# Kernel tuning notes

Hardware: AMD Instinct MI355X
Metric: run time of the kernel (lower is better)

Reference implementation:

```python
import jax, jax.numpy as jnp
import numpy as np

WS = (6, 12, 12)
STRIDE = (2, 2, 2)
NHEAD = 8
NPF = 32


def _pos_embed(Dm, Hm, Wm, pw):
    # Sine 3D position embedding, normalized, then 1x1x1 conv proj (pw: (C, 6*NPF)).
    eps = 1e-6
    two_pi = np.float32(2.0 * np.pi)
    z = jnp.arange(Dm, dtype=jnp.float32) / (Dm - 1 + eps) * two_pi
    y = jnp.arange(Hm, dtype=jnp.float32) / (Hm - 1 + eps) * two_pi
    x = jnp.arange(Wm, dtype=jnp.float32) / (Wm - 1 + eps) * two_pi
    zz, yy, xx = jnp.meshgrid(z, y, x, indexing='ij')
    dim_t = jnp.float32(10000.0) ** (jnp.arange(NPF, dtype=jnp.float32) / NPF)
    def emb(p):
        p = p[..., None] / dim_t                       # (D,H,W,NPF)
        return jnp.stack([jnp.sin(p), jnp.cos(p)], axis=-1).reshape(p.shape[:-1] + (2 * NPF,))
    pos = jnp.concatenate([emb(zz), emb(yy), emb(xx)], axis=-1)  # (D,H,W,6*NPF)
    return jnp.einsum('dhwf,cf->cdhw', pos, pw)        # (C,D,H,W)


def _pad_to_multiple(x, ws):
    B, C, D, H, W = x.shape
    pd, ph, pw = (-D) % ws[0], (-H) % ws[1], (-W) % ws[2]
    if pd or ph or pw:
        x = jnp.pad(x, ((0, 0), (0, 0), (0, pd), (0, ph), (0, pw)))
    return x


def _match(x, tgt):
    x = x[:, :, :tgt[0], :tgt[1], :tgt[2]]
    pd, ph, pw = tgt[0] - x.shape[2], tgt[1] - x.shape[3], tgt[2] - x.shape[4]
    if pd or ph or pw:
        x = jnp.pad(x, ((0, 0), (0, 0), (0, pd), (0, ph), (0, pw)))
    return x


def _partition(x, ws):
    # (B,C,D,H,W) -> (B, Nw, L, C) window tokens
    B, C, D, H, W = x.shape
    wd, wh, ww = ws
    x = x.reshape(B, C, D // wd, wd, H // wh, wh, W // ww, ww)
    x = x.transpose(0, 2, 4, 6, 3, 5, 7, 1)  # B,Dg,Hg,Wg,wd,wh,ww,C
    return x.reshape(B, (D // wd) * (H // wh) * (W // ww), wd * wh * ww, C)


def _reverse(tok, grid, ws, B, C):
    Dg, Hg, Wg = grid
    wd, wh, ww = ws
    x = tok.reshape(B, Dg, Hg, Wg, wd, wh, ww, C)
    x = x.transpose(0, 7, 1, 4, 2, 5, 3, 6)
    return x.reshape(B, C, Dg * wd, Hg * wh, Wg * ww)


def _wavelet_low_high(x):
    # Depthwise Haar DWT, kernel 2, stride 2 (D,H,W even). Returns LLL and sum of 7 high bands.
    B, C, D, H, W = x.shape
    s = np.float32(1.0 / np.sqrt(2.0))
    t = x.reshape(B, C, D // 2, 2, H // 2, 2, W // 2, 2)
    zL = (t[:, :, :, 0] + t[:, :, :, 1]) * s
    zH = (t[:, :, :, 1] - t[:, :, :, 0]) * s
    def sy(u):
        return (u[:, :, :, :, 0] + u[:, :, :, :, 1]) * s, (u[:, :, :, :, 1] - u[:, :, :, :, 0]) * s
    def sw(u):
        return (u[..., 0] + u[..., 1]) * s, (u[..., 1] - u[..., 0]) * s
    LL_, LH_ = sy(zL)
    HL_, HH_ = sy(zH)
    LLL, LLH = sw(LL_)
    LHL, LHH = sw(LH_)
    HLL, HLH = sw(HL_)
    HHL, HHH = sw(HH_)
    return LLL, LLH + LHL + LHH + HLL + HLH + HHL + HHH


def _forward(query_map, memory_map, pos_w, l_w1, l_b1, l_w2, l_b2,
             g_w1, g_b1, g_w2, g_b2, in_w, in_b, out_w, out_b, ln_w, ln_b):
    B, C, D, H, W = query_map.shape
    wd, wh, ww = WS
    sd, sh, sw_ = STRIDE
    q_pad = _pad_to_multiple(query_map, WS)
    m_pad = _pad_to_multiple(memory_map, WS)
    Dp, Hp, Wp = q_pad.shape[2:]
    qpos = _pos_embed(Dp, Hp, Wp, pos_w)[None]          # (1,C,Dp,Hp,Wp)
    # frequency-only KV pre (wavelet + MSCM gating)
    low, high = _wavelet_low_high(m_pad)
    Dk, Hk, Wk = low.shape[2:]
    low_t = low.reshape(B, C, -1).transpose(0, 2, 1)    # (B,Nk,C)
    high_t = high.reshape(B, C, -1).transpose(0, 2, 1)
    xm = high_t + low_t
    g = xm.mean(axis=1, keepdims=True)
    loc = jnp.maximum(xm @ l_w1.T + l_b1, 0.0) @ l_w2.T + l_b2
    glo = jnp.maximum(g @ g_w1.T + g_b1, 0.0) @ g_w2.T + g_b2
    wgate = jax.nn.sigmoid(loc + glo)
    fre = wgate * high_t + low_t
    kv_map = fre.transpose(0, 2, 1).reshape(B, C, Dk, Hk, Wk)
    kpos = _pos_embed(Dk, Hk, Wk, pos_w)[None]
    k_ws = (wd // sd, wh // sh, ww // sw_)
    nD, nH, nW = Dp // wd, Hp // wh, Wp // ww
    tgt = (nD * k_ws[0], nH * k_ws[1], nW * k_ws[2])
    kv_map = _match(kv_map, tgt)
    kpos = _match(kpos, tgt)
    q_tok = _partition(q_pad, WS)        # (B,Nw,Lq,C)
    qp_tok = _partition(qpos, WS)        # (1,Nw,Lq,C) broadcast over batch
    k_tok = _partition(kv_map, k_ws)     # (B,Nw,Lk,C)
    kp_tok = _partition(kpos, k_ws)
    qin = q_tok + qp_tok
    kin = k_tok + kp_tok
    dh = C // NHEAD
    Wq, Wk_, Wv = in_w[:C], in_w[C:2 * C], in_w[2 * C:]
    bq, bk, bv = in_b[:C], in_b[C:2 * C], in_b[2 * C:]
    Nw, Lq, Lk = q_tok.shape[1], q_tok.shape[2], k_tok.shape[2]
    q = (qin @ Wq.T + bq).reshape(B, Nw, Lq, NHEAD, dh)
    k = (kin @ Wk_.T + bk).reshape(B, Nw, Lk, NHEAD, dh)
    v = (k_tok @ Wv.T + bv).reshape(B, Nw, Lk, NHEAD, dh)
    scale = np.float32(1.0 / np.sqrt(dh))
    att = jax.nn.softmax(jnp.einsum('bnqhd,bnkhd->bnhqk', q, k) * scale, axis=-1)
    o = jnp.einsum('bnhqk,bnkhd->bnqhd', att, v).reshape(B, Nw, Lq, C)
    o = o @ out_w.T + out_b
    res = q_tok + o
    mu = res.mean(-1, keepdims=True)
    var = res.var(-1, keepdims=True)
    res = (res - mu) * jax.lax.rsqrt(var + 1e-5) * ln_w + ln_b
    out = _reverse(res, (nD, nH, nW), WS, B, C)
    return out[:, :, :D, :H, :W]


def setup_inputs() -> dict:
    key = jax.random.key(0)
    ks = jax.random.split(key, 9)
    C = 96
    shp = (1, C, 24, 96, 96)
    def w(k, s, sc=0.05):
        return jax.random.normal(k, s, jnp.float32) * sc
    return {
        'query_map': jax.random.normal(ks[0], shp, jnp.float32),
        'memory_map': jax.random.normal(ks[1], shp, jnp.float32),
        'pos_w': w(ks[2], (C, 6 * NPF)),
        'l_w1': w(ks[3], (C, C)), 'l_b1': jnp.zeros((C,), jnp.float32),
        'l_w2': w(ks[4], (C, C)), 'l_b2': jnp.zeros((C,), jnp.float32),
        'g_w1': w(ks[5], (C, C)), 'g_b1': jnp.zeros((C,), jnp.float32),
        'g_w2': w(ks[6], (C, C)), 'g_b2': jnp.zeros((C,), jnp.float32),
        'in_w': w(ks[7], (3 * C, C)), 'in_b': jnp.zeros((3 * C,), jnp.float32),
        'out_w': w(ks[8], (C, C)), 'out_b': jnp.zeros((C,), jnp.float32),
        'ln_w': jnp.ones((C,), jnp.float32), 'ln_b': jnp.zeros((C,), jnp.float32),
    }


def reference(query_map, memory_map, pos_w, l_w1, l_b1, l_w2, l_b2,
              g_w1, g_b1, g_w2, g_b2, in_w, in_b, out_w, out_b, ln_w, ln_b):
    return _forward(query_map, memory_map, pos_w, l_w1, l_b1, l_w2, l_b2,
                    g_w1, g_b1, g_w2, g_b2, in_w, in_b, out_w, out_b, ln_w, ln_b)
```

## Files before the change

kernel.cpp:

```cpp
#include <hip/hip_runtime.h>
#include <math.h>


using short8 = __attribute__((ext_vector_type(8))) short;
using f32x4  = __attribute__((ext_vector_type(4))) float;

__device__ __forceinline__ unsigned short f2bf(float f) {
  unsigned u = __builtin_bit_cast(unsigned, f);
  unsigned r = u + 0x7fffu + ((u >> 16) & 1u);
  return (unsigned short)(r >> 16);
}
__device__ __forceinline__ unsigned cvtpk(float a, float b) {
  unsigned r;
  asm("v_cvt_pk_bf16_f32 %0, %1, %2" : "=v"(r) : "v"(a), "v"(b));
  return r;
}
__device__ __forceinline__ short8 mk8(unsigned a, unsigned b, unsigned c, unsigned d) {
  union { unsigned u[4]; short8 s; } x;
  x.u[0] = a; x.u[1] = b; x.u[2] = c; x.u[3] = d;
  return x.s;
}

#define OFFB_TAB   0u
#define OFFB_GSUM  124416u
#define OFFB_GLO   124800u
#define OFFB_XM    125184u
#define OFFB_LOW   10742016u
#define OFFB_WQ    21358848u
#define OFFB_WK    21377280u
#define OFFB_WV    21395712u
#define OFFB_KP    21414144u
#define OFFB_VT    28754176u
#define OFFB_WOP   37142784u
#define MEMSET_OFF 21414144u
#define MEMSET_LEN 15753216u

__global__ void k_pos(const float* __restrict__ pos_w, float* __restrict__ tab) {
  int idx = blockIdx.x * 256 + threadIdx.x;
  if (idx >= 324 * 96) return;
  int c = idx % 96, p = idx / 96;
  int Dm, fo, pl;
  if (p < 24)       { Dm = 24; fo = 0;   pl = p; }
  else if (p < 120) { Dm = 96; fo = 64;  pl = p - 24; }
  else if (p < 216) { Dm = 96; fo = 128; pl = p - 120; }
  else if (p < 228) { Dm = 12; fo = 0;   pl = p - 216; }
  else if (p < 276) { Dm = 48; fo = 64;  pl = p - 228; }
  else              { Dm = 48; fo = 128; pl = p - 276; }
  float pos = (float)pl / ((float)(Dm - 1) + 1e-6f) * 6.2831853071795864769f;
  float acc = 0.f;
  for (int i = 0; i < 32; ++i) {
    float inv = powf(10000.f, -(float)i / 32.f);
    float a = pos * inv;
    acc += sinf(a) * pos_w[c * 192 + fo + 2 * i] + cosf(a) * pos_w[c * 192 + fo + 2 * i + 1];
  }
  tab[p * 96 + c] = acc;
}

__global__ void k_wprep(const float* __restrict__ in_w, const float* __restrict__ out_w,
                        unsigned short* __restrict__ wq, unsigned short* __restrict__ wk,
                        unsigned short* __restrict__ wv, unsigned short* __restrict__ wop2) {
  int i = blockIdx.x * 256 + threadIdx.x;
  if (i < 9216) {
    wq[i] = f2bf(in_w[i]);
    wk[i] = f2bf(in_w[9216 + i]);
    wv[i] = f2bf(in_w[18432 + i]);
    int co = i / 96, ci = i % 96;
    int hh = ci / 12, dd = ci % 12;
    wop2[co * 128 + (hh >> 1) * 32 + (dd >> 2) * 8 + (hh & 1) * 4 + (dd & 3)] = f2bf(out_w[i]);
  }
}

__global__ void k_wav(const float* __restrict__ mem, float* __restrict__ xm_g,
                      float* __restrict__ low_g, float* __restrict__ gsum) {
  __shared__ float sxm[96][49];
  __shared__ float slow[96][49];
  int dk = blockIdx.x / 48, hk = blockIdx.x % 48;
  int tid = threadIdx.x;
  for (int idx = tid; idx < 96 * 48; idx += 256) {
    int wk = idx % 48, c = idx / 48;
    const float* p = mem + (((size_t)c * 24 + 2 * dk) * 96 + 2 * hk) * 96 + 2 * wk;
    float s = p[0] + p[1] + p[96] + p[97];
    const float* p2 = p + 96 * 96;
    float x111 = p2[97];
    s += p2[0] + p2[1] + p2[96] + x111;
    sxm[c][wk] = 2.8284271247461903f * x111;
    slow[c][wk] = 0.35355339059327373f * s;
  }
  __syncthreads();
  int n0 = (dk * 48 + hk) * 48;
  for (int idx = tid; idx < 96 * 48; idx += 256) {
    int c = idx % 96, t = idx / 96;
    xm_g[(size_t)(n0 + t) * 96 + c] = sxm[c][t];
    low_g[(size_t)(n0 + t) * 96 + c] = slow[c][t];
  }
  if (tid < 96) {
    float a = 0.f;
    for (int t = 0; t < 48; ++t) a += sxm[tid][t];
    atomicAdd(&gsum[tid], a);
  }
}

__global__ void k_glo(const float* __restrict__ gsum, const float* __restrict__ g_w1,
                      const float* __restrict__ g_b1, const float* __restrict__ g_w2,
                      const float* __restrict__ g_b2, float* __restrict__ glo) {
  __shared__ float sg[96], sh[96];
  int t = threadIdx.x;
  if (t < 96) sg[t] = gsum[t] * (1.f / 27648.f);
  __syncthreads();
  if (t < 96) {
    float a = g_b1[t];
    for (int i = 0; i < 96; ++i) a += sg[i] * g_w1[t * 96 + i];
    sh[t] = fmaxf(a, 0.f);
  }
  __syncthreads();
  if (t < 96) {
    float a = g_b2[t];
    for (int i = 0; i < 96; ++i) a += sh[i] * g_w2[t * 96 + i];
    glo[t] = a;
  }
}

__global__ __launch_bounds__(512) void k_gate(
    const float* xm_g, const float* __restrict__ low_g,
    const float* __restrict__ l_w1, const float* __restrict__ l_b1,
    const float* __restrict__ l_w2, const float* __restrict__ l_b2,
    const float* __restrict__ glo, float* fre) {
  __shared__ float sxm[64][97];
  __shared__ float sH[64][97];
  __shared__ float sW1[96][97];
  __shared__ float sW2[96][97];
  __shared__ float sb1[96], sb2[96], sglo[96];
  int tid = threadIdx.x;
  int n0 = blockIdx.x * 64;
  for (int idx = tid; idx < 64 * 96; idx += 512) {
    int c = idx % 96, t = idx / 96;
    sxm[t][c] = xm_g[(size_t)(n0 + t) * 96 + c];
  }
  for (int idx = tid; idx < 96 * 96; idx += 512) {
    int ci = idx % 96, co = idx / 96;
    sW1[co][ci] = l_w1[idx];
    sW2[co][ci] = l_w2[idx];
  }
  if (tid < 96) { sb1[tid] = l_b1[tid]; sb2[tid] = l_b2[tid]; sglo[tid] = glo[tid]; }
  __syncthreads();
  for (int idx = tid; idx < 64 * 96; idx += 512) {
    int co = idx % 96, t = idx / 96;
    float a = sb1[co];
    for (int ci = 0; ci < 96; ++ci) a += sxm[t][ci] * sW1[co][ci];
    sH[t][co] = fmaxf(a, 0.f);
  }
  __syncthreads();
  for (int idx = tid; idx < 64 * 96; idx += 512) {
    int co = idx % 96, t = idx / 96;
    float a = sb2[co];
    for (int ci = 0; ci < 96; ++ci) a += sH[t][ci] * sW2[co][ci];
    float wg = 1.f / (1.f + expf(-(a + sglo[co])));
    size_t off = (size_t)(n0 + t) * 96 + co;
    float lo = low_g[off];
    fre[off] = wg * (sxm[t][co] - lo) + lo;
  }
}

__global__ __launch_bounds__(256) void k_kv2(
    const float* __restrict__ fre, const float* __restrict__ tab,
    const unsigned short* __restrict__ wk, const unsigned short* __restrict__ wv,
    const float* __restrict__ in_b,
    unsigned short* __restrict__ kp2, unsigned short* __restrict__ vtp) {
  __shared__ unsigned short sKin[112 * 104];
  __shared__ unsigned short sVin[112 * 104];
  __shared__ unsigned short sVt[4 * 96 * 18];
  int tid = threadIdx.x, nw = blockIdx.x;
  int dg = nw >> 6, hg = (nw >> 3) & 7, wg = nw & 7;
  for (int idx = tid; idx < 108 * 48; idx += 256) {
    int row = idx % 108, cop = idx / 108;
    int ld = row / 36, lh = (row / 6) % 6, lw = row % 6;
    int dk = dg * 3 + ld, hk = hg * 6 + lh, wk_ = wg * 6 + lw;
    int n = (dk * 48 + hk) * 48 + wk_;
    int co = cop * 2;
    float f0 = fre[(size_t)n * 96 + co], f1 = fre[(size_t)n * 96 + co + 1];
    float p0 = tab[20736 + dk * 96 + co] + tab[21888 + hk * 96 + co] + tab[26496 + wk_ * 96 + co];
    float p1 = tab[20736 + dk * 96 + co + 1] + tab[21888 + hk * 96 + co + 1] + tab[26496 + wk_ * 96 + co + 1];
    *(unsigned*)(&sKin[row * 104 + co]) = (unsigned)f2bf(f0 + p0) | ((unsigned)f2bf(f1 + p1) << 16);
    *(unsigned*)(&sVin[row * 104 + co]) = (unsigned)f2bf(f0) | ((unsigned)f2bf(f1) << 16);
  }
  __syncthreads();
  int wave = tid >> 6, lane = tid & 63, l15 = lane & 15, g = lane >> 4;
  for (int mtk = wave; mtk < 7; mtk += 4) {
    f32x4 DK[6], DV[6];
    #pragma unroll
    for (int nt = 0; nt < 6; ++nt) { DK[nt] = f32x4{0.f,0.f,0.f,0.f}; DV[nt] = f32x4{0.f,0.f,0.f,0.f}; }
    #pragma unroll
    for (int ks = 0; ks < 3; ++ks) {
      short8 ak = *(const short8*)(&sKin[(mtk * 16 + l15) * 104 + ks * 32 + g * 8]);
      short8 av = *(const short8*)(&sVin[(mtk * 16 + l15) * 104 + ks * 32 + g * 8]);
      #pragma unroll
      for (int nt = 0; nt < 6; ++nt) {
        short8 bk = *(const short8*)(&wk[(nt * 16 + l15) * 96 + ks * 32 + g * 8]);
        short8 bv = *(const short8*)(&wv[(nt * 16 + l15) * 96 + ks * 32 + g * 8]);
        DK[nt] = __builtin_amdgcn_mfma_f32_16x16x32_bf16(ak, bk, DK[nt], 0, 0, 0);
        DV[nt] = __builtin_amdgcn_mfma_f32_16x16x32_bf16(av, bv, DV[nt], 0, 0, 0);
      }
    }
    #pragma unroll
    for (int nt = 0; nt < 6; ++nt) {
      int co = nt * 16 + l15;
      float bk_ = in_b[96 + co], bv_ = in_b[192 + co];
      #pragma unroll
      for (int r = 0; r < 4; ++r) {
        int row = g * 4 + r;
        int kk = mtk * 16 + row;
        float vk = DK[nt][r] + bk_;
        float vk2 = __shfl_xor(vk, 1);
        if (!(l15 & 1) && kk < 108) {
          unsigned pk = (unsigned)f2bf(vk) | ((unsigned)f2bf(vk2) << 16);
          *(unsigned*)(&kp2[((size_t)(nw * 8 + co / 12) * 112 + kk) * 16 + co % 12]) = pk;
        }
        float vv = DV[nt][r] + bv_;
        sVt[wave * 1728 + co * 18 + row] = f2bf(vv);
      }
    }
    asm volatile("s_waitcnt lgkmcnt(0)" ::: "memory");
    int cnt = (mtk == 6) ? 12 : 16;
    for (int co = lane; co < 96; co += 64) {
      int hh = co / 12, dd = co % 12;
      size_t vrowb = ((size_t)(nw * 8 + hh) * 16 + dd) * 128;
      for (int kk2 = 0; kk2 < cnt; kk2 += 2) {
        unsigned v = *(const unsigned*)(&sVt[wave * 1728 + co * 18 + kk2]);
        int p = (mtk >> 1) * 32 + (kk2 >> 2) * 8 + (mtk & 1) * 4 + (kk2 & 3);
        *(unsigned*)(&vtp[vrowb + p]) = v;
      }
    }
  }
}

__device__ __forceinline__ f32x4 proc_head(
    const unsigned short* qtile, const unsigned short* kb, const unsigned short* vb,
    int h, int lane, int l15, int g) {
  short8 bq = short8{0,0,0,0,0,0,0,0};
  if (lane < 32) bq = *(const short8*)(&qtile[l15 * 136 + h * 16 + g * 8]);
  short8 ak[7];
  #pragma unroll
  for (int nt = 0; nt < 7; ++nt) {
    ak[nt] = short8{0,0,0,0,0,0,0,0};
    if (lane < 32) ak[nt] = *(const short8*)(&kb[((size_t)h * 112 + nt * 16 + l15) * 16 + g * 8]);
  }
  f32x4 S[7];
  #pragma unroll
  for (int nt = 0; nt < 7; ++nt)
    S[nt] = __builtin_amdgcn_mfma_f32_16x16x32_bf16(ak[nt], bq, f32x4{0.f,0.f,0.f,0.f}, 0, 0, 0);
  float mx = -3e38f;
  #pragma unroll
  for (int nt = 0; nt < 6; ++nt) {
    #pragma unroll
    for (int r = 0; r < 4; ++r) mx = fmaxf(mx, S[nt][r]);
  }
  if (g < 3) {
    #pragma unroll
    for (int r = 0; r < 4; ++r) mx = fmaxf(mx, S[6][r]);
  }
  mx = fmaxf(mx, __shfl_xor(mx, 16));
  mx = fmaxf(mx, __shfl_xor(mx, 32));
  float sum = 0.f;
  #pragma unroll
  for (int nt = 0; nt < 7; ++nt) {
    #pragma unroll
    for (int r = 0; r < 4; ++r) {
      float e = __expf(S[nt][r] - mx);
      if (nt == 6 && g == 3) e = 0.f;
      S[nt][r] = e;
      sum += e;
    }
  }
  sum += __shfl_xor(sum, 16);
  sum += __shfl_xor(sum, 32);
  float inv = 1.f / sum;
  short8 av[4];
  #pragma unroll
  for (int ks = 0; ks < 4; ++ks)
    av[ks] = *(const short8*)(&vb[((size_t)h * 16 + l15) * 128 + ks * 32 + g * 8]);
  f32x4 o = f32x4{0.f, 0.f, 0.f, 0.f};
  #pragma unroll
  for (int ks = 0; ks < 4; ++ks) {
    unsigned w0 = cvtpk(S[2 * ks][0], S[2 * ks][1]);
    unsigned w1 = cvtpk(S[2 * ks][2], S[2 * ks][3]);
    unsigned w2 = 0, w3 = 0;
    if (ks < 3) {
      w2 = cvtpk(S[2 * ks + 1][0], S[2 * ks + 1][1]);
      w3 = cvtpk(S[2 * ks + 1][2], S[2 * ks + 1][3]);
    }
    short8 pa = mk8(w0, w1, w2, w3);
    o = __builtin_amdgcn_mfma_f32_16x16x32_bf16(av[ks], pa, o, 0, 0, 0);
  }
  o[0] *= inv; o[1] *= inv; o[2] *= inv; o[3] *= inv;
  return o;
}

__global__ __launch_bounds__(256, 2) void k_att4(
    const float* __restrict__ query, const float* __restrict__ tab,
    const unsigned short* __restrict__ kp2, const unsigned short* __restrict__ vtp,
    const unsigned short* __restrict__ wq, const unsigned short* __restrict__ wop2,
    const float* __restrict__ in_b, const float* __restrict__ out_b,
    const float* __restrict__ ln_w, const float* __restrict__ ln_b,
    float* __restrict__ out) {
  __shared__ __align__(16) unsigned char smem[34816];
  int tid = threadIdx.x;
  int nw = blockIdx.x, part = blockIdx.y;
  int dg = nw >> 6, hg = (nw >> 3) & 7, wg = nw & 7;
  int wave = tid >> 6, lane = tid & 63, l15 = lane & 15, g = lane >> 4;
  unsigned char* wbase = smem + wave * 8704;
  unsigned short* qtile = (unsigned short*)wbase;
  unsigned short* sPq   = qtile + 2176;
  int wid = part * 4 + wave;

  for (int c = lane; c < 544; c += 64)
    *(int4*)(wbase + c * 16) = int4{0, 0, 0, 0};
  asm volatile("s_waitcnt lgkmcnt(0)" ::: "memory");

  const float scale = 0.28867513459481287f;
  float biasq[6];
  #pragma unroll
  for (int nt = 0; nt < 6; ++nt) biasq[nt] = in_b[nt * 16 + l15];
  const unsigned short* kb = kp2 + (size_t)nw * 8 * 112 * 16;
  const unsigned short* vb = vtp + (size_t)nw * 8 * 16 * 128;

  for (int mt = wid; mt < 54; mt += 16) {
    for (int c = lane; c < 16 * 48; c += 64) {
      int row = c & 15, cop = c >> 4;
      int co = cop * 2;
      int l = mt * 16 + row;
      int ld = l / 144, lh = (l / 12) % 12, lw = l % 12;
      int d = dg * 6 + ld, h = hg * 12 + lh, w = wg * 12 + lw;
      size_t qoff = (((size_t)co * 24 + d) * 96 + h) * 96 + w;
      float v0 = query[qoff] + tab[d * 96 + co] + tab[2304 + h * 96 + co] + tab[11520 + w * 96 + co];
      float v1 = query[qoff + 221184] + tab[d * 96 + co + 1] + tab[2304 + h * 96 + co + 1] + tab[11520 + w * 96 + co + 1];
      *(unsigned*)(&sPq[row * 136 + co]) = (unsigned)f2bf(v0) | ((unsigned)f2bf(v1) << 16);
    }
    asm volatile("s_waitcnt lgkmcnt(0)" ::: "memory");
    {
      f32x4 QD[6];
      #pragma unroll
      for (int nt = 0; nt < 6; ++nt) QD[nt] = f32x4{0.f, 0.f, 0.f, 0.f};
      #pragma unroll
      for (int ks = 0; ks < 3; ++ks) {
        short8 a = *(const short8*)(&sPq[l15 * 136 + ks * 32 + g * 8]);
        #pragma unroll
        for (int nt = 0; nt < 6; ++nt) {
          short8 bw = *(const short8*)(&wq[(nt * 16 + l15) * 96 + ks * 32 + g * 8]);
          QD[nt] = __builtin_amdgcn_mfma_f32_16x16x32_bf16(a, bw, QD[nt], 0, 0, 0);
        }
      }
      #pragma unroll
      for (int nt = 0; nt < 6; ++nt) {
        int co = nt * 16 + l15;
        #pragma unroll
        for (int r = 0; r < 4; ++r) {
          float v = (QD[nt][r] + biasq[nt]) * scale;
          float v2 = __shfl_xor(v, 1);
          if (!(l15 & 1)) {
            int row = g * 4 + r;
            unsigned pk = (unsigned)f2bf(v) | ((unsigned)f2bf(v2) << 16);
            *(unsigned*)(&qtile[row * 136 + (co / 12) * 16 + co % 12]) = pk;
          }
        }
      }
    }
    asm volatile("s_waitcnt lgkmcnt(0)" ::: "memory");
    f32x4 R[6];
    #pragma unroll
    for (int nt = 0; nt < 6; ++nt) R[nt] = f32x4{0.f, 0.f, 0.f, 0.f};
    #pragma unroll
    for (int hp = 0; hp < 4; ++hp) {
      f32x4 oA = proc_head(qtile, kb, vb, 2 * hp, lane, l15, g);
      f32x4 oB = proc_head(qtile, kb, vb, 2 * hp + 1, lane, l15, g);
      short8 pb = mk8(cvtpk(oA[0], oA[1]), cvtpk(oA[2], oA[3]),
                      cvtpk(oB[0], oB[1]), cvtpk(oB[2], oB[3]));
      #pragma unroll
      for (int nt = 0; nt < 6; ++nt) {
        short8 aw = *(const short8*)(&wop2[(nt * 16 + l15) * 128 + hp * 32 + g * 8]);
        R[nt] = __builtin_amdgcn_mfma_f32_16x16x32_bf16(aw, pb, R[nt], 0, 0, 0);
      }
    }
    {
      int l = mt * 16 + l15;
      int ld = l / 144, lh = (l / 12) % 12, lw = l % 12;
      int d = dg * 6 + ld, h_ = hg * 12 + lh, w_ = wg * 12 + lw;
      size_t sp = ((size_t)d * 96 + h_) * 96 + w_;
      float s = 0.f, s2 = 0.f;
      #pragma unroll
      for (int nt = 0; nt < 6; ++nt) {
        #pragma unroll
        for (int r = 0; r < 4; ++r) {
          int co = nt * 16 + 4 * g + r;
          float v = R[nt][r] + out_b[co] + query[(size_t)co * 221184 + sp];
          R[nt][r] = v;
          s += v; s2 += v * v;
        }
      }
      s += __shfl_xor(s, 16); s2 += __shfl_xor(s2, 16);
      s += __shfl_xor(s, 32); s2 += __shfl_xor(s2, 32);
      float mu = s * (1.f / 96.f);
      float var = s2 * (1.f / 96.f) - mu * mu;
      float rstd = rsqrtf(var + 1e-5f);
      #pragma unroll
      for (int nt = 0; nt < 6; ++nt) {
        #pragma unroll
        for (int r = 0; r < 4; ++r) {
          int co = nt * 16 + 4 * g + r;
          out[(size_t)co * 221184 + sp] = (R[nt][r] - mu) * rstd * ln_w[co] + ln_b[co];
        }
      }
    }
  }
}

extern "C" void kernel_launch(void* const* d_in, const int* in_sizes, int n_in,
                              void* d_out, int out_size, void* d_ws, size_t ws_size,
                              hipStream_t stream) {
  const float* query = (const float*)d_in[0];
  const float* mem   = (const float*)d_in[1];
  const float* pos_w = (const float*)d_in[2];
  const float* l_w1  = (const float*)d_in[3];
  const float* l_b1  = (const float*)d_in[4];
  const float* l_w2  = (const float*)d_in[5];
  const float* l_b2  = (const float*)d_in[6];
  const float* g_w1  = (const float*)d_in[7];
  const float* g_b1  = (const float*)d_in[8];
  const float* g_w2  = (const float*)d_in[9];
  const float* g_b2  = (const float*)d_in[10];
  const float* in_w  = (const float*)d_in[11];
  const float* in_b  = (const float*)d_in[12];
  const float* out_w = (const float*)d_in[13];
  const float* out_b = (const float*)d_in[14];
  const float* ln_w  = (const float*)d_in[15];
  const float* ln_b  = (const float*)d_in[16];
  unsigned char* ws = (unsigned char*)d_ws;
  float* tab  = (float*)(ws + OFFB_TAB);
  float* gsum = (float*)(ws + OFFB_GSUM);
  float* glo  = (float*)(ws + OFFB_GLO);
  float* xm   = (float*)(ws + OFFB_XM);
  float* low  = (float*)(ws + OFFB_LOW);
  unsigned short* wq   = (unsigned short*)(ws + OFFB_WQ);
  unsigned short* wk   = (unsigned short*)(ws + OFFB_WK);
  unsigned short* wv   = (unsigned short*)(ws + OFFB_WV);
  unsigned short* kp2  = (unsigned short*)(ws + OFFB_KP);
  unsigned short* vtp  = (unsigned short*)(ws + OFFB_VT);
  unsigned short* wop2 = (unsigned short*)(ws + OFFB_WOP);

  hipMemsetAsync(gsum, 0, 96 * sizeof(float), stream);
  hipMemsetAsync(ws + MEMSET_OFF, 0, MEMSET_LEN, stream);
  k_pos<<<(324 * 96 + 255) / 256, 256, 0, stream>>>(pos_w, tab);
  k_wprep<<<36, 256, 0, stream>>>(in_w, out_w, wq, wk, wv, wop2);
  k_wav<<<576, 256, 0, stream>>>(mem, xm, low, gsum);
  k_glo<<<1, 128, 0, stream>>>(gsum, g_w1, g_b1, g_w2, g_b2, glo);
  k_gate<<<432, 512, 0, stream>>>(xm, low, l_w1, l_b1, l_w2, l_b2, glo, xm);
  k_kv2<<<256, 256, 0, stream>>>(xm, tab, wk, wv, in_b, kp2, vtp);
  k_att4<<<dim3(256, 4), 256, 0, stream>>>(query, tab, kp2, vtp, wq, wop2, in_b, out_b,
                                           ln_w, ln_b, (float*)d_out);
}
```

Measured before the change: 455.6 us.

## Run local gating MLP on bf16 MFMA instead of scalar fp32 loops

Replaces the scalar fp32 shared-memory gating MLP with a bf16 MFMA kernel. Each block handles 108 tokens in 16-row tiles, keeping both 96x96 layers in MFMA accumulators and passing the hidden activations through LDS as bf16. The l_w1/l_w2 weights are pre-converted to bf16 in the weight-prep kernel, and k_pos swaps powf for a precomputed __expf. This removes a heavy FP32 FMA loop, at the cost of bf16 rounding in the gate computation and only 256 blocks with uneven wave work (7 row tiles spread over 4 waves).

```diff
diff --git a/kernel.cpp b/kernel.cpp
--- a/kernel.cpp
+++ b/kernel.cpp
@@ -32,6 +32,8 @@
 #define OFFB_KP    21414144u
 #define OFFB_VT    28754176u
 #define OFFB_WOP   37142784u
+#define OFFB_WG1   37167360u
+#define OFFB_WG2   37185792u
 #define MEMSET_OFF 21414144u
 #define MEMSET_LEN 15753216u
 
@@ -49,7 +51,7 @@
   float pos = (float)pl / ((float)(Dm - 1) + 1e-6f) * 6.2831853071795864769f;
   float acc = 0.f;
   for (int i = 0; i < 32; ++i) {
-    float inv = powf(10000.f, -(float)i / 32.f);
+    float inv = __expf((float)i * -0.2878231366242558f);
     float a = pos * inv;
     acc += sinf(a) * pos_w[c * 192 + fo + 2 * i] + cosf(a) * pos_w[c * 192 + fo + 2 * i + 1];
   }
@@ -57,13 +59,17 @@
 }
 
 __global__ void k_wprep(const float* __restrict__ in_w, const float* __restrict__ out_w,
+                        const float* __restrict__ l_w1, const float* __restrict__ l_w2,
                         unsigned short* __restrict__ wq, unsigned short* __restrict__ wk,
-                        unsigned short* __restrict__ wv, unsigned short* __restrict__ wop2) {
+                        unsigned short* __restrict__ wv, unsigned short* __restrict__ wop2,
+                        unsigned short* __restrict__ wg1, unsigned short* __restrict__ wg2) {
   int i = blockIdx.x * 256 + threadIdx.x;
   if (i < 9216) {
     wq[i] = f2bf(in_w[i]);
     wk[i] = f2bf(in_w[9216 + i]);
     wv[i] = f2bf(in_w[18432 + i]);
+    wg1[i] = f2bf(l_w1[i]);
+    wg2[i] = f2bf(l_w2[i]);
     int co = i / 96, ci = i % 96;
     int hh = ci / 12, dd = ci % 12;
     wop2[co * 128 + (hh >> 1) * 32 + (dd >> 2) * 8 + (hh & 1) * 4 + (dd & 3)] = f2bf(out_w[i]);
@@ -120,44 +126,83 @@
   }
 }
 
-__global__ __launch_bounds__(512) void k_gate(
+__global__ __launch_bounds__(256) void k_gate2(
     const float* xm_g, const float* __restrict__ low_g,
-    const float* __restrict__ l_w1, const float* __restrict__ l_b1,
-    const float* __restrict__ l_w2, const float* __restrict__ l_b2,
+    const unsigned short* __restrict__ wg1, const unsigned short* __restrict__ wg2,
+    const float* __restrict__ l_b1, const float* __restrict__ l_b2,
     const float* __restrict__ glo, float* fre) {
-  __shared__ float sxm[64][97];
-  __shared__ float sH[64][97];
-  __shared__ float sW1[96][97];
-  __shared__ float sW2[96][97];
-  __shared__ float sb1[96], sb2[96], sglo[96];
+  __shared__ unsigned short sXin[112 * 104];
+  __shared__ unsigned short sH[112 * 104];
   int tid = threadIdx.x;
-  int n0 = blockIdx.x * 64;
-  for (int idx = tid; idx < 64 * 96; idx += 512) {
-    int c = idx % 96, t = idx / 96;
-    sxm[t][c] = xm_g[(size_t)(n0 + t) * 96 + c];
-  }
-  for (int idx = tid; idx < 96 * 96; idx += 512) {
-    int ci = idx % 96, co = idx / 96;
-    sW1[co][ci] = l_w1[idx];
-    sW2[co][ci] = l_w2[idx];
-  }
-  if (tid < 96) { sb1[tid] = l_b1[tid]; sb2[tid] = l_b2[tid]; sglo[tid] = glo[tid]; }
+  int n0 = blockIdx.x * 108;
+  for (int idx = tid; idx < 112 * 48; idx += 256) {
+    int row = idx % 112, cop = idx / 112;
+    int co = cop * 2;
+    unsigned pk = 0;
+    if (row < 108) {
+      float f0 = xm_g[(size_t)(n0 + row) * 96 + co];
+      float f1 = xm_g[(size_t)(n0 + row) * 96 + co + 1];
+      pk = (unsigned)f2bf(f0) | ((unsigned)f2bf(f1) << 16);
+    }
+    *(unsigned*)(&sXin[row * 104 + co]) = pk;
+  }
   __syncthreads();
-  for (int idx = tid; idx < 64 * 96; idx += 512) {
-    int co = idx % 96, t = idx / 96;
-    float a = sb1[co];
-    for (int ci = 0; ci < 96; ++ci) a += sxm[t][ci] * sW1[co][ci];
-    sH[t][co] = fmaxf(a, 0.f);
-  }
-  __syncthreads();
-  for (int idx = tid; idx < 64 * 96; idx += 512) {
-    int co = idx % 96, t = idx / 96;
-    float a = sb2[co];
-    for (int ci = 0; ci < 96; ++ci) a += sH[t][ci] * sW2[co][ci];
-    float wg = 1.f / (1.f + expf(-(a + sglo[co])));
-    size_t off = (size_t)(n0 + t) * 96 + co;
-    float lo = low_g[off];
-    fre[off] = wg * (sxm[t][co] - lo) + lo;
+  int wave = tid >> 6, lane = tid & 63, l15 = lane & 15, g = lane >> 4;
+  for (int mtk = wave; mtk < 7; mtk += 4) {
+    f32x4 D[6];
+    #pragma unroll
+    for (int nt = 0; nt < 6; ++nt) D[nt] = f32x4{0.f, 0.f, 0.f, 0.f};
+    #pragma unroll
+    for (int ks = 0; ks < 3; ++ks) {
+      short8 a = *(const short8*)(&sXin[(mtk * 16 + l15) * 104 + ks * 32 + g * 8]);
+      #pragma unroll
+      for (int nt = 0; nt < 6; ++nt) {
+        short8 b = *(const short8*)(&wg1[(nt * 16 + l15) * 96 + ks * 32 + g * 8]);
+        D[nt] = __builtin_amdgcn_mfma_f32_16x16x32_bf16(a, b, D[nt], 0, 0, 0);
+      }
+    }
+    #pragma unroll
+    for (int nt = 0; nt < 6; ++nt) {
+      int co = nt * 16 + l15;
+      float b1v = l_b1[co];
+      #pragma unroll
+      for (int r = 0; r < 4; ++r) {
+        float h = fmaxf(D[nt][r] + b1v, 0.f);
+        float h2 = __shfl_xor(h, 1);
+        if (!(l15 & 1)) {
+          int row = mtk * 16 + g * 4 + r;
+          *(unsigned*)(&sH[row * 104 + co]) = (unsigned)f2bf(h) | ((unsigned)f2bf(h2) << 16);
+        }
+      }
+    }
+    asm volatile("s_waitcnt lgkmcnt(0)" ::: "memory");
+    f32x4 A[6];
+    #pragma unroll
+    for (int nt = 0; nt < 6; ++nt) A[nt] = f32x4{0.f, 0.f, 0.f, 0.f};
+    #pragma unroll
+    for (int ks = 0; ks < 3; ++ks) {
+      short8 a = *(const short8*)(&sH[(mtk * 16 + l15) * 104 + ks * 32 + g * 8]);
+      #pragma unroll
+      for (int nt = 0; nt < 6; ++nt) {
+        short8 b = *(const short8*)(&wg2[(nt * 16 + l15) * 96 + ks * 32 + g * 8]);
+        A[nt] = __builtin_amdgcn_mfma_f32_16x16x32_bf16(a, b, A[nt], 0, 0, 0);
+      }
+    }
+    #pragma unroll
+    for (int nt = 0; nt < 6; ++nt) {
+      int co = nt * 16 + l15;
+      float gb = l_b2[co] + glo[co];
+      #pragma unroll
+      for (int r = 0; r < 4; ++r) {
+        int row = mtk * 16 + g * 4 + r;
+        if (row < 108) {
+          size_t off = (size_t)(n0 + row) * 96 + co;
+          float wgv = 1.f / (1.f + __expf(-(A[nt][r] + gb)));
+          float xv = xm_g[off], lo = low_g[off];
+          fre[off] = wgv * (xv - lo) + lo;
+        }
+      }
+    }
   }
 }
 
@@ -445,14 +490,16 @@
   unsigned short* kp2  = (unsigned short*)(ws + OFFB_KP);
   unsigned short* vtp  = (unsigned short*)(ws + OFFB_VT);
   unsigned short* wop2 = (unsigned short*)(ws + OFFB_WOP);
+  unsigned short* wg1  = (unsigned short*)(ws + OFFB_WG1);
+  unsigned short* wg2  = (unsigned short*)(ws + OFFB_WG2);
 
   hipMemsetAsync(gsum, 0, 96 * sizeof(float), stream);
   hipMemsetAsync(ws + MEMSET_OFF, 0, MEMSET_LEN, stream);
   k_pos<<<(324 * 96 + 255) / 256, 256, 0, stream>>>(pos_w, tab);
-  k_wprep<<<36, 256, 0, stream>>>(in_w, out_w, wq, wk, wv, wop2);
+  k_wprep<<<36, 256, 0, stream>>>(in_w, out_w, l_w1, l_w2, wq, wk, wv, wop2, wg1, wg2);
   k_wav<<<576, 256, 0, stream>>>(mem, xm, low, gsum);
   k_glo<<<1, 128, 0, stream>>>(gsum, g_w1, g_b1, g_w2, g_b2, glo);
-  k_gate<<<432, 512, 0, stream>>>(xm, low, l_w1, l_b1, l_w2, l_b2, glo, xm);
+  k_gate2<<<256, 256, 0, stream>>>(xm, low, wg1, wg2, l_b1, l_b2, glo, xm);
   k_kv2<<<256, 256, 0, stream>>>(xm, tab, wk, wv, in_b, kp2, vtp);
   k_att4<<<dim3(256, 4), 256, 0, stream>>>(query, tab, kp2, vtp, wq, wop2, in_b, out_b,
                                            ln_w, ln_b, (float*)d_out);
```

New measurement: 389.9 us, median of 2. 1.17x faster.
